# Kernel tuning notes

Measured on AMD Instinct MI355X. Metric: run time of the kernel, lower is better.

Reference implementation:

```python
import jax, jax.numpy as jnp
import numpy as np

B, T, C = 1, 2048, 1024
HS = 64
H = C // HS
EPS_GN = 0.00064


def _fwd(x, v_first, x_prev, init_state, x_r, x_w, x_k, x_v, x_a, x_g,
         w0, w1, w2, a0, a1, a2, v0, v1, v2, g1, g2,
         k_k, k_a, r_k, Wr, Wk, Wv, Wo, ln_w, ln_b, cu_seqlens):
    # token shift: previous token, sequence starts replaced by cached state x_prev
    xx = jnp.concatenate([jnp.zeros((1, 1, C), x.dtype), x[:, :-1, :]], axis=1)
    xx = xx.at[0, cu_seqlens[:-1], :].set(x_prev)
    xx = xx - x
    xr = x + xx * x_r
    xw = x + xx * x_w
    xk = x + xx * x_k
    xv = x + xx * x_v
    xa = x + xx * x_a
    xg = x + xx * x_g
    r = xr @ Wr.T
    # log-decay, strictly negative: w = -exp(-softplus(-z) - 0.5)
    w = -jnp.exp(-jax.nn.softplus(-(w0 + jnp.tanh(xw @ w1) @ w2)) - 0.5)
    k = xk @ Wk.T
    v = xv @ Wv.T
    # layer_id != 0: mix toward first-layer value
    v = v + (v_first - v) * jax.nn.sigmoid(v0 + (xv @ v1) @ v2)
    a = jax.nn.sigmoid(a0 + (xa @ a1) @ a2)
    g = jax.nn.sigmoid(xg @ g1) @ g2
    kk = (k * k_k).reshape(B, T, H, HS)
    kk = kk / jnp.maximum(jnp.linalg.norm(kk, axis=-1, keepdims=True), 1e-12)
    k = k * (1.0 + (a - 1.0) * k_a)
    r4 = r.reshape(B, T, H, HS)
    w4 = w.reshape(B, T, H, HS)
    k4 = k.reshape(B, T, H, HS)
    v4 = v.reshape(B, T, H, HS)
    a4 = a.reshape(B, T, H, HS)
    aa = -kk
    bb = kk * a4

    # RWKV-7 selective-decay linear RNN (chunk_rwkv7 semantics):
    #   S_t = S_{t-1} diag(exp(w_t)) + (S_{t-1} a_t) b_t^T + v_t k_t^T ; o_t = S_t r_t
    def step(S, ts):
        r_t, w_t, k_t, v_t, a_t, b_t = ts  # each [H,HS]
        sa = jnp.einsum('hvj,hj->hv', S, a_t)
        S = S * jnp.exp(w_t)[:, None, :] + sa[:, :, None] * b_t[:, None, :] \
            + v_t[:, :, None] * k_t[:, None, :]
        o = jnp.einsum('hvk,hk->hv', S, r_t)
        return S, o

    _, y = jax.lax.scan(step, init_state, (r4[0], w4[0], k4[0], v4[0], aa[0], bb[0]))
    # GroupNorm with num_groups=H over channels, eps=0.00064
    y = y.reshape(B * T, H, HS)
    mu = y.mean(-1, keepdims=True)
    var = ((y - mu) ** 2).mean(-1, keepdims=True)
    yn = (y - mu) / jnp.sqrt(var + EPS_GN)
    yn = yn * ln_w.reshape(H, HS) + ln_b.reshape(H, HS)
    xo = yn.reshape(B, T, C)
    # per-head bonus term
    xo = xo + ((r4 * k4 * r_k).sum(-1, keepdims=True) * v4).reshape(B, T, C)
    return (xo * g) @ Wo.T


def setup_inputs():
    keys = jax.random.split(jax.random.key(0), 32)
    it = iter(range(32))
    def nrm(shape, s=0.02):
        return jax.random.normal(keys[next(it)], shape, dtype=jnp.float32) * s
    inp = {}
    inp['x'] = jax.random.normal(keys[next(it)], (B, T, C), jnp.float32)
    inp['v_first'] = jax.random.normal(keys[next(it)], (B, T, C), jnp.float32)
    inp['x_prev'] = jax.random.normal(keys[next(it)], (1, C), jnp.float32)
    inp['init_state'] = jnp.zeros((H, HS, HS), jnp.float32)
    for nm in ['x_r', 'x_w', 'x_k', 'x_v', 'x_a', 'x_g', 'w0', 'a0', 'v0', 'k_k', 'k_a']:
        inp[nm] = nrm((C,))
    inp['w1'] = nrm((C, 64)); inp['w2'] = nrm((64, C))
    inp['a1'] = nrm((C, 64)); inp['a2'] = nrm((64, C))
    inp['v1'] = nrm((C, 32)); inp['v2'] = nrm((32, C))
    inp['g1'] = nrm((C, 128)); inp['g2'] = nrm((128, C))
    inp['r_k'] = nrm((H, HS))
    inp['Wr'] = nrm((C, C)); inp['Wk'] = nrm((C, C))
    inp['Wv'] = nrm((C, C)); inp['Wo'] = nrm((C, C))
    inp['ln_w'] = jnp.ones((C,), jnp.float32)
    inp['ln_b'] = jnp.zeros((C,), jnp.float32)
    inp['cu_seqlens'] = jnp.array([0, T], dtype=jnp.int32)
    return inp


def reference(x, v_first, x_prev, init_state, x_r, x_w, x_k, x_v, x_a, x_g,
              w0, w1, w2, a0, a1, a2, v0, v1, v2, g1, g2,
              k_k, k_a, r_k, Wr, Wk, Wv, Wo, ln_w, ln_b, cu_seqlens):
    return _fwd(x, v_first, x_prev, init_state, x_r, x_w, x_k, x_v, x_a, x_g,
                w0, w1, w2, a0, a1, a2, v0, v1, v2, g1, g2,
                k_k, k_a, r_k, Wr, Wk, Wv, Wo, ln_w, ln_b, cu_seqlens)
```

## Files before the change

kernel.cpp:

```cpp
#include <hip/hip_runtime.h>

#define T_LEN 2048
#define C_DIM 1024
#define PAIR_F 768
#define NCH 32
#define CPAIR 32

#define AS1 __attribute__((address_space(1)))
#define AS3 __attribute__((address_space(3)))

typedef __attribute__((ext_vector_type(8))) short bf8_t;
typedef __attribute__((ext_vector_type(4))) float f4_t;
typedef __attribute__((ext_vector_type(2))) float f2_t;

static __device__ __forceinline__ float sigf(float x) {
    return 1.f / (1.f + __expf(-x));
}
static __device__ __forceinline__ unsigned short f2bf(float f) {
    unsigned u = __float_as_uint(f);
    u += 0x7fff + ((u >> 16) & 1);
    return (unsigned short)(u >> 16);
}

static __device__ __forceinline__ float red16(float x) {
    int xi;
    xi = __builtin_amdgcn_mov_dpp(__float_as_int(x), 0x128, 0xf, 0xf, true);
    x += __int_as_float(xi);
    xi = __builtin_amdgcn_mov_dpp(__float_as_int(x), 0x124, 0xf, 0xf, true);
    x += __int_as_float(xi);
    xi = __builtin_amdgcn_mov_dpp(__float_as_int(x), 0x122, 0xf, 0xf, true);
    x += __int_as_float(xi);
    xi = __builtin_amdgcn_mov_dpp(__float_as_int(x), 0x121, 0xf, 0xf, true);
    x += __int_as_float(xi);
    return x;
}
static __device__ __forceinline__ float red64(float x) {
    x = red16(x);
    x += __shfl_xor(x, 16);
    x += __shfl_xor(x, 32);
    return x;
}

static __device__ __forceinline__ f2_t f2bc(float s) { return (f2_t){s, s}; }
static __device__ __forceinline__ f2_t fma2(f2_t a, f2_t b, f2_t c) {
    return __builtin_elementwise_fma(a, b, c);
}
static __device__ __forceinline__ f2_t lo2(const float4& v) { return (f2_t){v.x, v.y}; }
static __device__ __forceinline__ f2_t hi2(const float4& v) { return (f2_t){v.z, v.w}; }

static __device__ __forceinline__ float dot4pk(f2_t Sl, f2_t Sh, const float4& A) {
    f2_t m = Sl * lo2(A);
    m = fma2(Sh, hi2(A), m);
    return m.x + m.y;
}

__global__ __launch_bounds__(256) void wcvtall(
    const float* __restrict__ Wr, const float* __restrict__ Wk,
    const float* __restrict__ Wv, const float* __restrict__ Wo,
    const float* __restrict__ w1, const float* __restrict__ a1,
    const float* __restrict__ v1, const float* __restrict__ g1,
    unsigned short* __restrict__ dst, unsigned short* __restrict__ lw16)
{
    const int b = blockIdx.x;
    if (b < 4096) {
        const size_t idx = ((size_t)b * 256 + threadIdx.x) * 4;
        const int sel = (int)(idx >> 20);
        const float* src = sel == 0 ? Wr : sel == 1 ? Wk : sel == 2 ? Wv : Wo;
        float4 v = *(const float4*)(src + (idx & 0xFFFFF));
        ushort4 o = {f2bf(v.x), f2bf(v.y), f2bf(v.z), f2bf(v.w)};
        *(ushort4*)(dst + idx) = o;
        return;
    }
    const int row = b - 4096;
    const float* src; int Kh, i; unsigned short* dl;
    if (row < 64)       { src = w1; Kh = 64;  i = row;       dl = lw16 + (size_t)row * 1024; }
    else if (row < 128) { src = a1; Kh = 64;  i = row - 64;  dl = lw16 + (size_t)row * 1024; }
    else if (row < 160) { src = v1; Kh = 32;  i = row - 128; dl = lw16 + (size_t)(row - 128 + 128) * 1024; }
    else                { src = g1; Kh = 128; i = row - 160; dl = lw16 + (size_t)(row - 160 + 192) * 1024; }
    const int c0 = threadIdx.x * 4;
#pragma unroll
    for (int u = 0; u < 4; ++u)
        dl[c0 + u] = f2bf(src[(size_t)(c0 + u) * Kh + i]);
}

__global__ __launch_bounds__(256) void xcvt(
    const float* __restrict__ x, const float* __restrict__ xprev,
    const float* __restrict__ x_r, const float* __restrict__ x_k,
    const float* __restrict__ x_v, const float* __restrict__ x_w,
    const float* __restrict__ x_a, const float* __restrict__ x_g,
    unsigned short* __restrict__ xr16, unsigned short* __restrict__ xk16,
    unsigned short* __restrict__ xv16, unsigned short* __restrict__ xw16,
    unsigned short* __restrict__ xa16, unsigned short* __restrict__ xg16)
{
    const int t = blockIdx.x;
    const int c0 = threadIdx.x * 4;
    const size_t base = (size_t)t * C_DIM + c0;
    float4 xv = *(const float4*)(x + base);
    float4 pv = (t == 0) ? *(const float4*)(xprev + c0)
                         : *(const float4*)(x + base - C_DIM);
    float4 dx = {pv.x - xv.x, pv.y - xv.y, pv.z - xv.z, pv.w - xv.w};
#define MIXOUT(mixp, dstp)                                                    \
    {                                                                          \
        float4 mv = *(const float4*)(mixp + c0);                               \
        ushort4 o = {f2bf(xv.x + dx.x * mv.x), f2bf(xv.y + dx.y * mv.y),       \
                     f2bf(xv.z + dx.z * mv.z), f2bf(xv.w + dx.w * mv.w)};      \
        *(ushort4*)(dstp + base) = o;                                          \
    }
    MIXOUT(x_r, xr16) MIXOUT(x_k, xk16) MIXOUT(x_v, xv16)
    MIXOUT(x_w, xw16) MIXOUT(x_a, xa16) MIXOUT(x_g, xg16)
#undef MIXOUT
}

static __device__ __forceinline__ void gemm_core(
    const unsigned short* __restrict__ A, const unsigned short* __restrict__ W,
    float* __restrict__ out)
{
    __shared__ unsigned short Ab[2][128 * 32];
    __shared__ unsigned short Bb[2][64 * 32];
    const int tid = threadIdx.x;
    const int lane = tid & 63;
    const int w = tid >> 6;
    const int n0 = blockIdx.x * 64;
    const int t0 = blockIdx.y * 128;
    const int wm = (w & 1) * 64;
    const int wn = (w >> 1) * 32;
    const int srow = lane >> 2;
    const int scol = (lane & 3) * 8;

    f4_t acc[4][2];
#pragma unroll
    for (int i = 0; i < 4; ++i)
#pragma unroll
        for (int j = 0; j < 2; ++j)
            acc[i][j] = (f4_t){0.f, 0.f, 0.f, 0.f};

#pragma unroll
    for (int s = 0; s < 2; ++s) {
        const int i = 2 * w + s;
        __builtin_amdgcn_global_load_lds(
            (const AS1 unsigned int*)(A + (size_t)(t0 + i * 16 + srow) * 1024 + scol),
            (AS3 unsigned int*)(&Ab[0][i * 512 + lane * 8]), 16, 0, 0);
    }
    __builtin_amdgcn_global_load_lds(
        (const AS1 unsigned int*)(W + (size_t)(n0 + w * 16 + srow) * 1024 + scol),
        (AS3 unsigned int*)(&Bb[0][w * 512 + lane * 8]), 16, 0, 0);

    const int mrow = lane & 15;
    const int kq = (lane >> 4) * 8;
    for (int k0 = 0; k0 < 1024; k0 += 32) {
        const int cur = (k0 >> 5) & 1, nxt = cur ^ 1;
        __syncthreads();
        if (k0 + 32 < 1024) {
            const int k1 = k0 + 32;
#pragma unroll
            for (int s = 0; s < 2; ++s) {
                const int i = 2 * w + s;
                __builtin_amdgcn_global_load_lds(
                    (const AS1 unsigned int*)(A + (size_t)(t0 + i * 16 + srow) * 1024 + k1 + scol),
                    (AS3 unsigned int*)(&Ab[nxt][i * 512 + lane * 8]), 16, 0, 0);
            }
            __builtin_amdgcn_global_load_lds(
                (const AS1 unsigned int*)(W + (size_t)(n0 + w * 16 + srow) * 1024 + k1 + scol),
                (AS3 unsigned int*)(&Bb[nxt][w * 512 + lane * 8]), 16, 0, 0);
        }
        bf8_t af[4], bfr[2];
#pragma unroll
        for (int i = 0; i < 4; ++i)
            af[i] = *(const bf8_t*)(&Ab[cur][(wm + 16 * i + mrow) * 32 + kq]);
#pragma unroll
        for (int j = 0; j < 2; ++j)
            bfr[j] = *(const bf8_t*)(&Bb[cur][(wn + 16 * j + mrow) * 32 + kq]);
#pragma unroll
        for (int i = 0; i < 4; ++i)
#pragma unroll
            for (int j = 0; j < 2; ++j)
                acc[i][j] = __builtin_amdgcn_mfma_f32_16x16x32_bf16(
                    af[i], bfr[j], acc[i][j], 0, 0, 0);
    }
    const int crow = (lane >> 4) * 4;
    const int ccol = lane & 15;
#pragma unroll
    for (int i = 0; i < 4; ++i)
#pragma unroll
        for (int j = 0; j < 2; ++j)
#pragma unroll
            for (int u = 0; u < 4; ++u)
                out[(size_t)(t0 + wm + 16 * i + crow + u) * 1024
                    + n0 + wn + 16 * j + ccol] = acc[i][j][u];
}

__global__ __launch_bounds__(256) void gemm_bf16_3(
    const unsigned short* __restrict__ xr, const unsigned short* __restrict__ xk,
    const unsigned short* __restrict__ xv,
    const unsigned short* __restrict__ Wr, const unsigned short* __restrict__ Wk,
    const unsigned short* __restrict__ Wv,
    float* __restrict__ rB, float* __restrict__ kB, float* __restrict__ vB)
{
    const int z = blockIdx.z;
    const unsigned short* A = z == 0 ? xr : z == 1 ? xk : xv;
    const unsigned short* W = z == 0 ? Wr : z == 1 ? Wk : Wv;
    float* out = z == 0 ? rB : z == 1 ? kB : vB;
    gemm_core(A, W, out);
}

__global__ __launch_bounds__(256) void gemm_bf16(
    const unsigned short* __restrict__ A, const unsigned short* __restrict__ W,
    float* __restrict__ out)
{
    gemm_core(A, W, out);
}

__global__ __launch_bounds__(256) void lora1m(
    const unsigned short* __restrict__ xw, const unsigned short* __restrict__ xa,
    const unsigned short* __restrict__ xv, const unsigned short* __restrict__ xg,
    const unsigned short* __restrict__ lw16,
    float* __restrict__ hw, float* __restrict__ ha, float* __restrict__ hv,
    float* __restrict__ hg)
{
    const int z = blockIdx.z;
    const unsigned short* A = z == 0 ? xw : z == 1 ? xa : z == 2 ? xv : xg;
    const unsigned short* W = lw16 + (size_t)(z == 0 ? 0 : z == 1 ? 64 : z == 2 ? 128 : 192) * 1024;
    float* out = z == 0 ? hw : z == 1 ? ha : z == 2 ? hv : hg;
    const int N  = z == 3 ? 128 : z == 2 ? 32 : 64;
    const int Ns = z == 3 ? 128 : 64;
    const int n0 = blockIdx.x * 64;
    if (n0 >= Ns) return;

    __shared__ unsigned short Ab[2][128 * 32];
    __shared__ unsigned short Bb[2][64 * 32];
    const int tid = threadIdx.x;
    const int lane = tid & 63;
    const int w = tid >> 6;
    const int t0 = blockIdx.y * 128;
    const int wm = (w & 1) * 64;
    const int wn = (w >> 1) * 32;
    const int srow = lane >> 2;
    const int scol = (lane & 3) * 8;

    f4_t acc[4][2];
#pragma unroll
    for (int i = 0; i < 4; ++i)
#pragma unroll
        for (int j = 0; j < 2; ++j)
            acc[i][j] = (f4_t){0.f, 0.f, 0.f, 0.f};

#pragma unroll
    for (int s = 0; s < 2; ++s) {
        const int i = 2 * w + s;
        __builtin_amdgcn_global_load_lds(
            (const AS1 unsigned int*)(A + (size_t)(t0 + i * 16 + srow) * 1024 + scol),
            (AS3 unsigned int*)(&Ab[0][i * 512 + lane * 8]), 16, 0, 0);
    }
    __builtin_amdgcn_global_load_lds(
        (const AS1 unsigned int*)(W + (size_t)(n0 + w * 16 + srow) * 1024 + scol),
        (AS3 unsigned int*)(&Bb[0][w * 512 + lane * 8]), 16, 0, 0);

    const int mrow = lane & 15;
    const int kq = (lane >> 4) * 8;
    for (int k0 = 0; k0 < 1024; k0 += 32) {
        const int cur = (k0 >> 5) & 1, nxt = cur ^ 1;
        __syncthreads();
        if (k0 + 32 < 1024) {
            const int k1 = k0 + 32;
#pragma unroll
            for (int s = 0; s < 2; ++s) {
                const int i = 2 * w + s;
                __builtin_amdgcn_global_load_lds(
                    (const AS1 unsigned int*)(A + (size_t)(t0 + i * 16 + srow) * 1024 + k1 + scol),
                    (AS3 unsigned int*)(&Ab[nxt][i * 512 + lane * 8]), 16, 0, 0);
            }
            __builtin_amdgcn_global_load_lds(
                (const AS1 unsigned int*)(W + (size_t)(n0 + w * 16 + srow) * 1024 + k1 + scol),
                (AS3 unsigned int*)(&Bb[nxt][w * 512 + lane * 8]), 16, 0, 0);
        }
        bf8_t af[4], bfr[2];
#pragma unroll
        for (int i = 0; i < 4; ++i)
            af[i] = *(const bf8_t*)(&Ab[cur][(wm + 16 * i + mrow) * 32 + kq]);
#pragma unroll
        for (int j = 0; j < 2; ++j)
            bfr[j] = *(const bf8_t*)(&Bb[cur][(wn + 16 * j + mrow) * 32 + kq]);
#pragma unroll
        for (int i = 0; i < 4; ++i)
#pragma unroll
            for (int j = 0; j < 2; ++j)
                acc[i][j] = __builtin_amdgcn_mfma_f32_16x16x32_bf16(
                    af[i], bfr[j], acc[i][j], 0, 0, 0);
    }
    const int crow = (lane >> 4) * 4;
    const int ccol = lane & 15;
#pragma unroll
    for (int i = 0; i < 4; ++i)
#pragma unroll
        for (int j = 0; j < 2; ++j) {
            const int col = n0 + wn + 16 * j + ccol;
            if (col < N) {
#pragma unroll
                for (int u = 0; u < 4; ++u) {
                    float vv = acc[i][j][u];
                    if (z == 0) vv = tanhf(vv);
                    else if (z == 3) vv = sigf(vv);
                    out[(size_t)(t0 + wm + 16 * i + crow + u) * N + col] = vv;
                }
            }
        }
}

#define TOK 4
__global__ __launch_bounds__(256) void lora2f(
    const float* __restrict__ hwB, const float* __restrict__ haB,
    const float* __restrict__ hvB, const float* __restrict__ hgB,
    const float* __restrict__ w2, const float* __restrict__ a2,
    const float* __restrict__ v2, const float* __restrict__ g2,
    const float* __restrict__ w0, const float* __restrict__ a0,
    const float* __restrict__ v0,
    const float* __restrict__ k_k, const float* __restrict__ k_a,
    const float* __restrict__ v_first, const float* __restrict__ rB,
    float* __restrict__ kB, float* __restrict__ vB, float* __restrict__ gB,
    float* __restrict__ pk)
{
    const int tid = threadIdx.x;
    const int t0 = blockIdx.y * TOK;
    const int i  = blockIdx.x * 256 + tid;
    const int h  = i >> 6;
    const int j  = i & 63;

    float av[TOK], ew[TOK], vf[TOK];
    {
        float acc[TOK];
        const float b0 = a0[i];
#pragma unroll
        for (int tt = 0; tt < TOK; ++tt) acc[tt] = b0;
        for (int jj = 0; jj < 64; jj += 4) {
            const float q0 = a2[(size_t)(jj + 0) * C_DIM + i];
            const float q1 = a2[(size_t)(jj + 1) * C_DIM + i];
            const float q2 = a2[(size_t)(jj + 2) * C_DIM + i];
            const float q3 = a2[(size_t)(jj + 3) * C_DIM + i];
#pragma unroll
            for (int tt = 0; tt < TOK; ++tt) {
                float4 h4 = *(const float4*)(haB + (size_t)(t0 + tt) * 64 + jj);
                acc[tt] = fmaf(h4.x, q0, acc[tt]);
                acc[tt] = fmaf(h4.y, q1, acc[tt]);
                acc[tt] = fmaf(h4.z, q2, acc[tt]);
                acc[tt] = fmaf(h4.w, q3, acc[tt]);
            }
        }
#pragma unroll
        for (int tt = 0; tt < TOK; ++tt) av[tt] = sigf(acc[tt]);
    }
    {
        float acc[TOK];
        const float b0 = w0[i];
#pragma unroll
        for (int tt = 0; tt < TOK; ++tt) acc[tt] = b0;
        for (int jj = 0; jj < 64; jj += 4) {
            const float q0 = w2[(size_t)(jj + 0) * C_DIM + i];
            const float q1 = w2[(size_t)(jj + 1) * C_DIM + i];
            const float q2 = w2[(size_t)(jj + 2) * C_DIM + i];
            const float q3 = w2[(size_t)(jj + 3) * C_DIM + i];
#pragma unroll
            for (int tt = 0; tt < TOK; ++tt) {
                float4 h4 = *(const float4*)(hwB + (size_t)(t0 + tt) * 64 + jj);
                acc[tt] = fmaf(h4.x, q0, acc[tt]);
                acc[tt] = fmaf(h4.y, q1, acc[tt]);
                acc[tt] = fmaf(h4.z, q2, acc[tt]);
                acc[tt] = fmaf(h4.w, q3, acc[tt]);
            }
        }
#pragma unroll
        for (int tt = 0; tt < TOK; ++tt)
            ew[tt] = __expf(-0.6065306597126334f * sigf(acc[tt]));
    }
    {
        float acc[TOK];
        const float b0 = v0[i];
#pragma unroll
        for (int tt = 0; tt < TOK; ++tt) acc[tt] = b0;
        for (int jj = 0; jj < 32; jj += 4) {
            const float q0 = v2[(size_t)(jj + 0) * C_DIM + i];
            const float q1 = v2[(size_t)(jj + 1) * C_DIM + i];
            const float q2 = v2[(size_t)(jj + 2) * C_DIM + i];
            const float q3 = v2[(size_t)(jj + 3) * C_DIM + i];
#pragma unroll
            for (int tt = 0; tt < TOK; ++tt) {
                float4 h4 = *(const float4*)(hvB + (size_t)(t0 + tt) * 32 + jj);
                acc[tt] = fmaf(h4.x, q0, acc[tt]);
                acc[tt] = fmaf(h4.y, q1, acc[tt]);
                acc[tt] = fmaf(h4.z, q2, acc[tt]);
                acc[tt] = fmaf(h4.w, q3, acc[tt]);
            }
        }
#pragma unroll
        for (int tt = 0; tt < TOK; ++tt) {
            const size_t gi = (size_t)(t0 + tt) * C_DIM + i;
            const float s = sigf(acc[tt]);
            const float vr = vB[gi];
            vf[tt] = vr + (v_first[gi] - vr) * s;
            vB[gi] = vf[tt];
        }
    }
    {
        float acc[TOK];
#pragma unroll
        for (int tt = 0; tt < TOK; ++tt) acc[tt] = 0.f;
        for (int jj = 0; jj < 128; jj += 4) {
            const float q0 = g2[(size_t)(jj + 0) * C_DIM + i];
            const float q1 = g2[(size_t)(jj + 1) * C_DIM + i];
            const float q2 = g2[(size_t)(jj + 2) * C_DIM + i];
            const float q3 = g2[(size_t)(jj + 3) * C_DIM + i];
#pragma unroll
            for (int tt = 0; tt < TOK; ++tt) {
                float4 h4 = *(const float4*)(hgB + (size_t)(t0 + tt) * 128 + jj);
                acc[tt] = fmaf(h4.x, q0, acc[tt]);
                acc[tt] = fmaf(h4.y, q1, acc[tt]);
                acc[tt] = fmaf(h4.z, q2, acc[tt]);
                acc[tt] = fmaf(h4.w, q3, acc[tt]);
            }
        }
#pragma unroll
        for (int tt = 0; tt < TOK; ++tt)
            gB[(size_t)(t0 + tt) * C_DIM + i] = acc[tt];
    }
    const float kkw = k_k[i], kaw = k_a[i];
    const size_t pbase = (size_t)h * 1024 * PAIR_F;
    for (int pt = 0; pt < TOK / 2; ++pt) {
        float r_[2], e_[2], kf_[2], v_[2], aa_[2], bb_[2];
#pragma unroll
        for (int u = 0; u < 2; ++u) {
            const int tt = 2 * pt + u;
            const size_t gi = (size_t)(t0 + tt) * C_DIM + i;
            const float kraw = kB[gi];
            const float kn = kraw * kkw;
            const float ss = red64(kn * kn);
            const float sc = 1.f / fmaxf(sqrtf(ss), 1e-12f);
            const float kk = kn * sc;
            const float a_ = av[tt];
            const float kf = kraw * (1.f + (a_ - 1.f) * kaw);
            kB[gi] = kf;
            r_[u] = rB[gi];
            e_[u] = ew[tt];
            kf_[u] = kf;
            v_[u] = vf[tt];
            aa_[u] = -kk;
            bb_[u] = kk * a_;
        }
        const float E   = e_[0] * e_[1];
        const float A2e = e_[0] * aa_[1];
        const float B1e = bb_[0] * e_[1];
        const float K1e = kf_[0] * e_[1];
        const float R1e = e_[0] * r_[0];
        const float cba = red64(bb_[0] * aa_[1]);
        const float cka = red64(kf_[0] * aa_[1]);
        const float cbr = red64(bb_[0] * r_[0]);
        const float ckr = red64(kf_[0] * r_[0]);
        const float cbr2  = red64(B1e * r_[1]);
        const float ckr2  = red64(K1e * r_[1]);
        const float cb2r2 = red64(bb_[1] * r_[1]);
        const float ck2r2 = red64(kf_[1] * r_[1]);
        float* p = pk + pbase + (size_t)(blockIdx.y * (TOK / 2) + pt) * PAIR_F;
        p[j]        = E;
        p[64 + j]   = aa_[0];
        p[128 + j]  = A2e;
        p[192 + j]  = B1e;
        p[256 + j]  = K1e;
        p[320 + j]  = bb_[1];
        p[384 + j]  = kf_[1];
        p[448 + j]  = R1e;
        p[512 + j]  = E * r_[1];
        p[576 + 2 * j]     = v_[0];
        p[576 + 2 * j + 1] = v_[1];
        if (j == 0) {
            p[704] = cba;  p[705] = cka;  p[706] = cbr;  p[707] = ckr;
            p[708] = cbr2; p[709] = ckr2; p[710] = cb2r2; p[711] = ck2r2;
        }
    }
}

struct SlotPC {
    float4 E, A1, A2e, B1e, K1e, B2, K2;
    float4 vva, vvb;
    float4 sc;
};

static __device__ __forceinline__ void slot_load_pc(
    SlotPC& K, const float* __restrict__ p, int j0, int rb2)
{
    K.E   = *(const float4*)(p + j0);
    K.A1  = *(const float4*)(p + 64 + j0);
    K.A2e = *(const float4*)(p + 128 + j0);
    K.B1e = *(const float4*)(p + 192 + j0);
    K.K1e = *(const float4*)(p + 256 + j0);
    K.B2  = *(const float4*)(p + 320 + j0);
    K.K2  = *(const float4*)(p + 384 + j0);
    K.vva = *(const float4*)(p + 576 + rb2);
    K.vvb = *(const float4*)(p + 576 + rb2 + 4);
    K.sc  = *(const float4*)(p + 704);
}

static __device__ __forceinline__ void pair_pc(
    f2_t* PSl, f2_t* PSh, f2_t* CSl, f2_t* CSh, const SlotPC& K)
{
    float pu1[4], pu2[4], cu1[4], cu2[4];
#pragma unroll
    for (int r = 0; r < 4; ++r) {
        pu1[r] = red16(dot4pk(PSl[r], PSh[r], K.A1));
        pu2[r] = red16(dot4pk(PSl[r], PSh[r], K.A2e));
        cu1[r] = red16(dot4pk(CSl[r], CSh[r], K.A1));
        cu2[r] = red16(dot4pk(CSl[r], CSh[r], K.A2e));
    }
#pragma unroll
    for (int r = 0; r < 4; ++r) {
        {
            const float sa1 = pu1[r];
            const float sa2 = fmaf(sa1, K.sc.x, pu2[r]);
            const f2_t sa1v = f2bc(sa1), sa2v = f2bc(sa2);
            f2_t nl = PSl[r] * lo2(K.E), nh = PSh[r] * hi2(K.E);
            nl = fma2(sa1v, lo2(K.B1e), nl); nh = fma2(sa1v, hi2(K.B1e), nh);
            nl = fma2(sa2v, lo2(K.B2), nl);  nh = fma2(sa2v, hi2(K.B2), nh);
            PSl[r] = nl; PSh[r] = nh;
        }
        {
            const float v1 = r == 0 ? K.vva.x : r == 1 ? K.vva.z
                           : r == 2 ? K.vvb.x : K.vvb.z;
            const float v2 = r == 0 ? K.vva.y : r == 1 ? K.vva.w
                           : r == 2 ? K.vvb.y : K.vvb.w;
            const float sa1 = cu1[r];
            const float sa2 = fmaf(v1, K.sc.y, fmaf(sa1, K.sc.x, cu2[r]));
            const f2_t sa1v = f2bc(sa1), sa2v = f2bc(sa2);
            const f2_t v1v = f2bc(v1), v2v = f2bc(v2);
            f2_t nl = CSl[r] * lo2(K.E), nh = CSh[r] * hi2(K.E);
            nl = fma2(sa1v, lo2(K.B1e), nl); nh = fma2(sa1v, hi2(K.B1e), nh);
            nl = fma2(v1v, lo2(K.K1e), nl);  nh = fma2(v1v, hi2(K.K1e), nh);
            nl = fma2(sa2v, lo2(K.B2), nl);  nh = fma2(sa2v, hi2(K.B2), nh);
            nl = fma2(v2v, lo2(K.K2), nl);   nh = fma2(v2v, hi2(K.K2), nh);
            CSl[r] = nl; CSh[r] = nh;
        }
    }
}

__global__ __launch_bounds__(64, 1) void pc_fused(
    const float* __restrict__ pk, float* __restrict__ Pbuf,
    float* __restrict__ Cbuf)
{
    const int b = blockIdx.x;
    const int h = b & 15;
    const int w = (b >> 4) & 3;
    const int c = b >> 6;
    const int l = threadIdx.x;
    const int q = l >> 4;
    const int j0 = (l & 15) * 4;
    const int rbase = w * 16 + q * 4;
    const int rb2 = 2 * rbase;
    const float* hbase = pk + ((size_t)h * 1024 + (size_t)c * CPAIR) * PAIR_F;

    f2_t PSl[4], PSh[4], CSl[4], CSh[4];
#pragma unroll
    for (int r = 0; r < 4; ++r) {
        const int row = rbase + r;
        PSl[r] = (f2_t){j0 == row ? 1.f : 0.f, j0 + 1 == row ? 1.f : 0.f};
        PSh[r] = (f2_t){j0 + 2 == row ? 1.f : 0.f, j0 + 3 == row ? 1.f : 0.f};
        CSl[r] = (f2_t){0.f, 0.f};
        CSh[r] = (f2_t){0.f, 0.f};
    }

    SlotPC s0, s1, s2, s3;
    slot_load_pc(s0, hbase + 0 * PAIR_F, j0, rb2);
    slot_load_pc(s1, hbase + 1 * PAIR_F, j0, rb2);
    slot_load_pc(s2, hbase + 2 * PAIR_F, j0, rb2);
    slot_load_pc(s3, hbase + 3 * PAIR_F, j0, rb2);
    __builtin_amdgcn_sched_barrier(0);

    for (int i = 0; i < CPAIR - 4; i += 4) {
        const float* pl = hbase + (size_t)(i + 4) * PAIR_F;
        pair_pc(PSl, PSh, CSl, CSh, s0); slot_load_pc(s0, pl + 0 * PAIR_F, j0, rb2);
        __builtin_amdgcn_sched_barrier(0);
        pair_pc(PSl, PSh, CSl, CSh, s1); slot_load_pc(s1, pl + 1 * PAIR_F, j0, rb2);
        __builtin_amdgcn_sched_barrier(0);
        pair_pc(PSl, PSh, CSl, CSh, s2); slot_load_pc(s2, pl + 2 * PAIR_F, j0, rb2);
        __builtin_amdgcn_sched_barrier(0);
        pair_pc(PSl, PSh, CSl, CSh, s3); slot_load_pc(s3, pl + 3 * PAIR_F, j0, rb2);
        __builtin_amdgcn_sched_barrier(0);
    }
    pair_pc(PSl, PSh, CSl, CSh, s0);
    pair_pc(PSl, PSh, CSl, CSh, s1);
    pair_pc(PSl, PSh, CSl, CSh, s2);
    pair_pc(PSl, PSh, CSl, CSh, s3);

    const size_t cb64 = ((size_t)h * NCH + c) * 4096;
#pragma unroll
    for (int r = 0; r < 4; ++r) {
        *(float4*)(Pbuf + cb64 + (size_t)(rbase + r) * 64 + j0) =
            (float4){PSl[r].x, PSl[r].y, PSh[r].x, PSh[r].y};
        *(float4*)(Cbuf + cb64 + (size_t)(rbase + r) * 64 + j0) =
            (float4){CSl[r].x, CSl[r].y, CSh[r].x, CSh[r].y};
    }
}

__global__ __launch_bounds__(64) void combine(
    const float* __restrict__ Pbuf, float* __restrict__ CSbuf,
    const float* __restrict__ init_state)
{
    const int b = blockIdx.x;
    const int h = b & 15;
    const int g = b >> 4;
    const int l = threadIdx.x;
    const int vl = l >> 4;
    const int vidx = g * 4 + vl;
    const int j0 = (l & 15) * 4;
    __shared__ __align__(16) float Pl[64 * 64];
    __shared__ __align__(16) float sl[4 * 64];

    float4 s = *(const float4*)(init_state + h * 4096 + vidx * 64 + j0);
    for (int c = 0; c < NCH; ++c) {
        const size_t cbase = ((size_t)h * NCH + c) * 4096;
        float* cp = CSbuf + cbase + (size_t)vidx * 64 + j0;
        float4 Cv = *(const float4*)cp;
        *(float4*)cp = s;
        const float* Psrc = Pbuf + cbase;
#pragma unroll
        for (int t = 0; t < 16; ++t)
            *(float4*)(&Pl[t * 256 + l * 4]) = *(const float4*)(Psrc + t * 256 + l * 4);
        *(float4*)(&sl[vl * 64 + j0]) = s;
        __syncthreads();
        f2_t al = {Cv.x, Cv.y}, ah = {Cv.z, Cv.w};
        for (int k = 0; k < 64; ++k) {
            const float sk = sl[vl * 64 + k];
            float4 Pr = *(const float4*)(&Pl[k * 64 + j0]);
            al = fma2(f2bc(sk), lo2(Pr), al);
            ah = fma2(f2bc(sk), hi2(Pr), ah);
        }
        s = (float4){al.x, al.y, ah.x, ah.y};
        __syncthreads();
    }
}

struct SlotO {
    float4 E, A1, A2e, B1e, K1e, B2, K2, R1e, R2e;
    float4 vva, vvb;
    float4 sc, sc2;
};

static __device__ __forceinline__ void slot_load_o(
    SlotO& K, const float* __restrict__ p, int j0, int rb2)
{
    K.E   = *(const float4*)(p + j0);
    K.A1  = *(const float4*)(p + 64 + j0);
    K.A2e = *(const float4*)(p + 128 + j0);
    K.B1e = *(const float4*)(p + 192 + j0);
    K.K1e = *(const float4*)(p + 256 + j0);
    K.B2  = *(const float4*)(p + 320 + j0);
    K.K2  = *(const float4*)(p + 384 + j0);
    K.R1e = *(const float4*)(p + 448 + j0);
    K.R2e = *(const float4*)(p + 512 + j0);
    K.vva = *(const float4*)(p + 576 + rb2);
    K.vvb = *(const float4*)(p + 576 + rb2 + 4);
    K.sc  = *(const float4*)(p + 704);
    K.sc2 = *(const float4*)(p + 708);
}

static __device__ __forceinline__ void pair_out(
    f2_t* Sl, f2_t* Sh, const SlotO& K, float4& o1v, float4& o2v)
{
    float u1[4], u2[4], op[4], oz[4];
#pragma unroll
    for (int r = 0; r < 4; ++r) {
        u1[r] = red16(dot4pk(Sl[r], Sh[r], K.A1));
        u2[r] = red16(dot4pk(Sl[r], Sh[r], K.A2e));
        op[r] = red16(dot4pk(Sl[r], Sh[r], K.R1e));
        oz[r] = red16(dot4pk(Sl[r], Sh[r], K.R2e));
    }
    float o1a[4], o2a[4];
#pragma unroll
    for (int r = 0; r < 4; ++r) {
        const float v1 = r == 0 ? K.vva.x : r == 1 ? K.vva.z
                       : r == 2 ? K.vvb.x : K.vvb.z;
        const float v2 = r == 0 ? K.vva.y : r == 1 ? K.vva.w
                       : r == 2 ? K.vvb.y : K.vvb.w;
        const float sa1 = u1[r];
        const float sa2 = fmaf(v1, K.sc.y, fmaf(sa1, K.sc.x, u2[r]));
        o1a[r] = fmaf(v1, K.sc.w, fmaf(sa1, K.sc.z, op[r]));
        o2a[r] = fmaf(v2, K.sc2.w, fmaf(sa2, K.sc2.z,
                 fmaf(v1, K.sc2.y, fmaf(sa1, K.sc2.x, oz[r]))));
        const f2_t sa1v = f2bc(sa1), sa2v = f2bc(sa2);
        const f2_t v1v = f2bc(v1), v2v = f2bc(v2);
        f2_t nl = Sl[r] * lo2(K.E), nh = Sh[r] * hi2(K.E);
        nl = fma2(sa1v, lo2(K.B1e), nl); nh = fma2(sa1v, hi2(K.B1e), nh);
        nl = fma2(v1v, lo2(K.K1e), nl);  nh = fma2(v1v, hi2(K.K1e), nh);
        nl = fma2(sa2v, lo2(K.B2), nl);  nh = fma2(sa2v, hi2(K.B2), nh);
        nl = fma2(v2v, lo2(K.K2), nl);   nh = fma2(v2v, hi2(K.K2), nh);
        Sl[r] = nl; Sh[r] = nh;
    }
    o1v = (float4){o1a[0], o1a[1], o1a[2], o1a[3]};
    o2v = (float4){o2a[0], o2a[1], o2a[2], o2a[3]};
}

__global__ __launch_bounds__(64, 1) void out_scan(
    const float* __restrict__ pk, const float* __restrict__ Scbuf,
    float* __restrict__ y)
{
    const int b = blockIdx.x;
    const int h = b & 15;
    const int w = (b >> 4) & 3;
    const int c = b >> 6;
    const int l = threadIdx.x;
    const int q = l >> 4;
    const int j0 = (l & 15) * 4;
    const int rbase = w * 16 + q * 4;
    const int rb2 = 2 * rbase;
    const int cb = h * 64;
    const float* hbase = pk + ((size_t)h * 1024 + (size_t)c * CPAIR) * PAIR_F;
    const size_t cb64 = ((size_t)h * NCH + c) * 4096;

    f2_t Sl[4], Sh[4];
#pragma unroll
    for (int r = 0; r < 4; ++r) {
        float4 S4 = *(const float4*)(Scbuf + cb64 + (size_t)(rbase + r) * 64 + j0);
        Sl[r] = (f2_t){S4.x, S4.y};
        Sh[r] = (f2_t){S4.z, S4.w};
    }

    SlotO s0, s1;
    slot_load_o(s0, hbase + 0 * PAIR_F, j0, rb2);
    slot_load_o(s1, hbase + 1 * PAIR_F, j0, rb2);
    __builtin_amdgcn_sched_barrier(0);

    const bool wr = (l & 15) == 0;
    const int pi0 = c * CPAIR;
    float4 o1v, o2v;
#define OUT_STORE(pidx)                                                       \
    if (wr) {                                                                 \
        float* yp = y + (size_t)(2 * (pidx)) * C_DIM + cb + rbase;            \
        *(float4*)yp = o1v;                                                   \
        *(float4*)(yp + C_DIM) = o2v;                                         \
    }
    for (int i = 0; i < CPAIR - 2; i += 2) {
        pair_out(Sl, Sh, s0, o1v, o2v);
        slot_load_o(s0, hbase + (size_t)(i + 2) * PAIR_F, j0, rb2);
        __builtin_amdgcn_sched_barrier(0);
        OUT_STORE(pi0 + i)
        pair_out(Sl, Sh, s1, o1v, o2v);
        if (i + 3 < CPAIR)
            slot_load_o(s1, hbase + (size_t)(i + 3) * PAIR_F, j0, rb2);
        __builtin_amdgcn_sched_barrier(0);
        OUT_STORE(pi0 + i + 1)
    }
    pair_out(Sl, Sh, s0, o1v, o2v);
    OUT_STORE(pi0 + CPAIR - 2)
    pair_out(Sl, Sh, s1, o1v, o2v);
    OUT_STORE(pi0 + CPAIR - 1)
#undef OUT_STORE
}

__global__ __launch_bounds__(256) void gn_bonus(
    const float* __restrict__ y, const float* __restrict__ rb,
    const float* __restrict__ kb, const float* __restrict__ vb,
    const float* __restrict__ gb, const float* __restrict__ r_k,
    const float* __restrict__ lnw, const float* __restrict__ lnb,
    unsigned short* __restrict__ yg)
{
    const int t = blockIdx.x, tid = threadIdx.x;
    const int c0 = tid << 2;
    const size_t base = (size_t)t * C_DIM + c0;
    float4 yv = *(const float4*)(y + base);
    float sum = yv.x + yv.y + yv.z + yv.w;
    float ss  = yv.x * yv.x + yv.y * yv.y + yv.z * yv.z + yv.w * yv.w;
    float4 rv = *(const float4*)(rb + base);
    float4 kv = *(const float4*)(kb + base);
    float4 rkv = *(const float4*)(r_k + c0);
    float dot = rv.x * kv.x * rkv.x + rv.y * kv.y * rkv.y +
                rv.z * kv.z * rkv.z + rv.w * kv.w * rkv.w;
#pragma unroll
    for (int m = 1; m <= 8; m <<= 1) {
        sum += __shfl_xor(sum, m);
        ss  += __shfl_xor(ss, m);
        dot += __shfl_xor(dot, m);
    }
    const float mu = sum * 0.015625f;
    const float var = ss * 0.015625f - mu * mu;
    const float rstd = rsqrtf(var + 0.00064f);
    float4 wv = *(const float4*)(lnw + c0);
    float4 bv = *(const float4*)(lnb + c0);
    float4 vv = *(const float4*)(vb + base);
    float4 gv = *(const float4*)(gb + base);
    ushort4 o;
    o.x = f2bf(((yv.x - mu) * rstd * wv.x + bv.x + dot * vv.x) * gv.x);
    o.y = f2bf(((yv.y - mu) * rstd * wv.y + bv.y + dot * vv.y) * gv.y);
    o.z = f2bf(((yv.z - mu) * rstd * wv.z + bv.z + dot * vv.z) * gv.z);
    o.w = f2bf(((yv.w - mu) * rstd * wv.w + bv.w + dot * vv.w) * gv.w);
    *(ushort4*)(yg + base) = o;
}

extern "C" void kernel_launch(void* const* d_in, const int* in_sizes, int n_in,
                              void* d_out, int out_size, void* d_ws, size_t ws_size,
                              hipStream_t stream)
{
    (void)in_sizes; (void)n_in; (void)out_size; (void)ws_size;
    const float* x       = (const float*)d_in[0];
    const float* v_first = (const float*)d_in[1];
    const float* x_prev  = (const float*)d_in[2];
    const float* init_st = (const float*)d_in[3];
    const float* x_r = (const float*)d_in[4];
    const float* x_w = (const float*)d_in[5];
    const float* x_k = (const float*)d_in[6];
    const float* x_v = (const float*)d_in[7];
    const float* x_a = (const float*)d_in[8];
    const float* x_g = (const float*)d_in[9];
    const float* w0  = (const float*)d_in[10];
    const float* a0  = (const float*)d_in[11];
    const float* v0  = (const float*)d_in[12];
    const float* k_k = (const float*)d_in[13];
    const float* k_a = (const float*)d_in[14];
    const float* w1  = (const float*)d_in[15];
    const float* w2  = (const float*)d_in[16];
    const float* a1  = (const float*)d_in[17];
    const float* a2  = (const float*)d_in[18];
    const float* v1  = (const float*)d_in[19];
    const float* v2  = (const float*)d_in[20];
    const float* g1  = (const float*)d_in[21];
    const float* g2  = (const float*)d_in[22];
    const float* r_k = (const float*)d_in[23];
    const float* Wr  = (const float*)d_in[24];
    const float* Wk  = (const float*)d_in[25];
    const float* Wv  = (const float*)d_in[26];
    const float* Wo  = (const float*)d_in[27];
    const float* ln_w = (const float*)d_in[28];
    const float* ln_b = (const float*)d_in[29];

    float* out = (float*)d_out;
    float* ws  = (float*)d_ws;
    const size_t NE = (size_t)T_LEN * C_DIM;
    const size_t WE = (size_t)C_DIM * C_DIM;
    float* rB  = ws;
    float* kB  = ws + NE;
    float* vB  = ws + 2 * NE;
    float* gB  = ws + 3 * NE;
    float* hwB = ws + 4 * NE;
    float* haB = hwB + (size_t)T_LEN * 64;
    float* hvB = haB + (size_t)T_LEN * 64;
    float* hgB = hvB + (size_t)T_LEN * 32;
    float* pk  = ws + 4 * NE + NE / 2;
    unsigned short* b16 = (unsigned short*)(ws + 10 * NE + NE / 2);
    unsigned short* xr16 = b16;
    unsigned short* xk16 = b16 + NE;
    unsigned short* xv16 = b16 + 2 * NE;
    unsigned short* Wr16 = b16 + 3 * NE;
    unsigned short* Wk16 = Wr16 + WE;
    unsigned short* Wv16 = Wr16 + 2 * WE;
    unsigned short* Wo16 = Wr16 + 3 * WE;
    unsigned short* yg16 = b16 + 3 * NE + 4 * WE;
    unsigned short* lw16 = yg16 + NE;
    unsigned short* xw16 = (unsigned short*)pk;
    unsigned short* xa16 = xw16 + NE;
    unsigned short* xg16 = xw16 + 2 * NE;
    float* yB = (float*)xr16;
    float* Pbuf  = (float*)xr16;
    float* CSbuf = (float*)xv16;

    wcvtall<<<4384, 256, 0, stream>>>(Wr, Wk, Wv, Wo, w1, a1, v1, g1,
                                      Wr16, lw16);
    xcvt<<<T_LEN, 256, 0, stream>>>(x, x_prev, x_r, x_k, x_v, x_w, x_a, x_g,
                                    xr16, xk16, xv16, xw16, xa16, xg16);

    gemm_bf16_3<<<dim3(16, 16, 3), 256, 0, stream>>>(
        xr16, xk16, xv16, Wr16, Wk16, Wv16, rB, kB, vB);

    lora1m<<<dim3(2, 16, 4), 256, 0, stream>>>(
        xw16, xa16, xv16, xg16, lw16, hwB, haB, hvB, hgB);

    lora2f<<<dim3(4, T_LEN / TOK), 256, 0, stream>>>(
        hwB, haB, hvB, hgB, w2, a2, v2, g2, w0, a0, v0,
        k_k, k_a, v_first, rB, kB, vB, gB, pk);

    pc_fused<<<16 * 4 * NCH, 64, 0, stream>>>(pk, Pbuf, CSbuf);
    combine<<<256, 64, 0, stream>>>(Pbuf, CSbuf, init_st);
    out_scan<<<16 * 4 * NCH, 64, 0, stream>>>(pk, CSbuf, yB);

    gn_bonus<<<T_LEN, 256, 0, stream>>>(yB, rB, kB, vB, gB, r_k, ln_w, ln_b, yg16);
    gemm_bf16<<<dim3(16, 16), 256, 0, stream>>>(yg16, Wo16, out);
}
```

Measured before the change: 378.2 us.

## Move g-LoRA second projection from scalar FMA loop to bf16 MFMA GEMM

The sigmoid(xg@g1)@g2 projection is taken out of the fp32 scalar loop in lora2f and computed by a new bf16 MFMA GEMM kernel (K=128). lora1m now writes the hidden activation in bf16, and wcvtall gains extra blocks that transpose g2 and convert it to bf16. This cuts scalar FMA work and g2 reloads in lora2f, at the cost of one more kernel launch and bf16 rounding of the gate path.

```diff
diff --git a/kernel.cpp b/kernel.cpp
--- a/kernel.cpp
+++ b/kernel.cpp
@@ -59,7 +59,9 @@
     const float* __restrict__ Wv, const float* __restrict__ Wo,
     const float* __restrict__ w1, const float* __restrict__ a1,
     const float* __restrict__ v1, const float* __restrict__ g1,
-    unsigned short* __restrict__ dst, unsigned short* __restrict__ lw16)
+    const float* __restrict__ g2,
+    unsigned short* __restrict__ dst, unsigned short* __restrict__ lw16,
+    unsigned short* __restrict__ g2t16)
 {
     const int b = blockIdx.x;
     if (b < 4096) {
@@ -69,6 +71,13 @@
         float4 v = *(const float4*)(src + (idx & 0xFFFFF));
         ushort4 o = {f2bf(v.x), f2bf(v.y), f2bf(v.z), f2bf(v.w)};
         *(ushort4*)(dst + idx) = o;
+        return;
+    }
+    if (b >= 4384) {
+        const int rr = b - 4384;
+        const int i  = rr * 2 + (threadIdx.x >> 7);
+        const int c  = threadIdx.x & 127;
+        g2t16[(size_t)i * 128 + c] = f2bf(g2[(size_t)c * C_DIM + i]);
         return;
     }
     const int row = b - 4096;
@@ -210,17 +219,95 @@
     gemm_core(A, W, out);
 }
 
+__global__ __launch_bounds__(256) void gemm_g(
+    const unsigned short* __restrict__ A, const unsigned short* __restrict__ W,
+    float* __restrict__ out)
+{
+    __shared__ unsigned short Ab[2][128 * 32];
+    __shared__ unsigned short Bb[2][64 * 32];
+    const int tid = threadIdx.x;
+    const int lane = tid & 63;
+    const int w = tid >> 6;
+    const int n0 = blockIdx.x * 64;
+    const int t0 = blockIdx.y * 128;
+    const int wm = (w & 1) * 64;
+    const int wn = (w >> 1) * 32;
+    const int srow = lane >> 2;
+    const int scol = (lane & 3) * 8;
+
+    f4_t acc[4][2];
+#pragma unroll
+    for (int i = 0; i < 4; ++i)
+#pragma unroll
+        for (int j = 0; j < 2; ++j)
+            acc[i][j] = (f4_t){0.f, 0.f, 0.f, 0.f};
+
+#pragma unroll
+    for (int s = 0; s < 2; ++s) {
+        const int i = 2 * w + s;
+        __builtin_amdgcn_global_load_lds(
+            (const AS1 unsigned int*)(A + (size_t)(t0 + i * 16 + srow) * 128 + scol),
+            (AS3 unsigned int*)(&Ab[0][i * 512 + lane * 8]), 16, 0, 0);
+    }
+    __builtin_amdgcn_global_load_lds(
+        (const AS1 unsigned int*)(W + (size_t)(n0 + w * 16 + srow) * 128 + scol),
+        (AS3 unsigned int*)(&Bb[0][w * 512 + lane * 8]), 16, 0, 0);
+
+    const int mrow = lane & 15;
+    const int kq = (lane >> 4) * 8;
+    for (int k0 = 0; k0 < 128; k0 += 32) {
+        const int cur = (k0 >> 5) & 1, nxt = cur ^ 1;
+        __syncthreads();
+        if (k0 + 32 < 128) {
+            const int k1 = k0 + 32;
+#pragma unroll
+            for (int s = 0; s < 2; ++s) {
+                const int i = 2 * w + s;
+                __builtin_amdgcn_global_load_lds(
+                    (const AS1 unsigned int*)(A + (size_t)(t0 + i * 16 + srow) * 128 + k1 + scol),
+                    (AS3 unsigned int*)(&Ab[nxt][i * 512 + lane * 8]), 16, 0, 0);
+            }
+            __builtin_amdgcn_global_load_lds(
+                (const AS1 unsigned int*)(W + (size_t)(n0 + w * 16 + srow) * 128 + k1 + scol),
+                (AS3 unsigned int*)(&Bb[nxt][w * 512 + lane * 8]), 16, 0, 0);
+        }
+        bf8_t af[4], bfr[2];
+#pragma unroll
+        for (int i = 0; i < 4; ++i)
+            af[i] = *(const bf8_t*)(&Ab[cur][(wm + 16 * i + mrow) * 32 + kq]);
+#pragma unroll
+        for (int j = 0; j < 2; ++j)
+            bfr[j] = *(const bf8_t*)(&Bb[cur][(wn + 16 * j + mrow) * 32 + kq]);
+#pragma unroll
+        for (int i = 0; i < 4; ++i)
+#pragma unroll
+            for (int j = 0; j < 2; ++j)
+                acc[i][j] = __builtin_amdgcn_mfma_f32_16x16x32_bf16(
+                    af[i], bfr[j], acc[i][j], 0, 0, 0);
+    }
+    const int crow = (lane >> 4) * 4;
+    const int ccol = lane & 15;
+#pragma unroll
+    for (int i = 0; i < 4; ++i)
+#pragma unroll
+        for (int j = 0; j < 2; ++j)
+#pragma unroll
+            for (int u = 0; u < 4; ++u)
+                out[(size_t)(t0 + wm + 16 * i + crow + u) * 1024
+                    + n0 + wn + 16 * j + ccol] = acc[i][j][u];
+}
+
 __global__ __launch_bounds__(256) void lora1m(
     const unsigned short* __restrict__ xw, const unsigned short* __restrict__ xa,
     const unsigned short* __restrict__ xv, const unsigned short* __restrict__ xg,
     const unsigned short* __restrict__ lw16,
     float* __restrict__ hw, float* __restrict__ ha, float* __restrict__ hv,
-    float* __restrict__ hg)
+    unsigned short* __restrict__ hg16)
 {
     const int z = blockIdx.z;
     const unsigned short* A = z == 0 ? xw : z == 1 ? xa : z == 2 ? xv : xg;
     const unsigned short* W = lw16 + (size_t)(z == 0 ? 0 : z == 1 ? 64 : z == 2 ? 128 : 192) * 1024;
-    float* out = z == 0 ? hw : z == 1 ? ha : z == 2 ? hv : hg;
+    float* out = z == 0 ? hw : z == 1 ? ha : hv;
     const int N  = z == 3 ? 128 : z == 2 ? 32 : 64;
     const int Ns = z == 3 ? 128 : 64;
     const int n0 = blockIdx.x * 64;
@@ -298,9 +385,15 @@
 #pragma unroll
                 for (int u = 0; u < 4; ++u) {
                     float vv = acc[i][j][u];
-                    if (z == 0) vv = tanhf(vv);
-                    else if (z == 3) vv = sigf(vv);
-                    out[(size_t)(t0 + wm + 16 * i + crow + u) * N + col] = vv;
+                    if (z == 0) {
+                        vv = tanhf(vv);
+                        out[(size_t)(t0 + wm + 16 * i + crow + u) * N + col] = vv;
+                    } else if (z == 3) {
+                        vv = sigf(vv);
+                        hg16[(size_t)(t0 + wm + 16 * i + crow + u) * 128 + col] = f2bf(vv);
+                    } else {
+                        out[(size_t)(t0 + wm + 16 * i + crow + u) * N + col] = vv;
+                    }
                 }
             }
         }
@@ -309,14 +402,14 @@
 #define TOK 4
 __global__ __launch_bounds__(256) void lora2f(
     const float* __restrict__ hwB, const float* __restrict__ haB,
-    const float* __restrict__ hvB, const float* __restrict__ hgB,
+    const float* __restrict__ hvB,
     const float* __restrict__ w2, const float* __restrict__ a2,
-    const float* __restrict__ v2, const float* __restrict__ g2,
+    const float* __restrict__ v2,
     const float* __restrict__ w0, const float* __restrict__ a0,
     const float* __restrict__ v0,
     const float* __restrict__ k_k, const float* __restrict__ k_a,
     const float* __restrict__ v_first, const float* __restrict__ rB,
-    float* __restrict__ kB, float* __restrict__ vB, float* __restrict__ gB,
+    float* __restrict__ kB, float* __restrict__ vB,
     float* __restrict__ pk)
 {
     const int tid = threadIdx.x;
@@ -398,28 +491,6 @@
             vf[tt] = vr + (v_first[gi] - vr) * s;
             vB[gi] = vf[tt];
         }
-    }
-    {
-        float acc[TOK];
-#pragma unroll
-        for (int tt = 0; tt < TOK; ++tt) acc[tt] = 0.f;
-        for (int jj = 0; jj < 128; jj += 4) {
-            const float q0 = g2[(size_t)(jj + 0) * C_DIM + i];
-            const float q1 = g2[(size_t)(jj + 1) * C_DIM + i];
-            const float q2 = g2[(size_t)(jj + 2) * C_DIM + i];
-            const float q3 = g2[(size_t)(jj + 3) * C_DIM + i];
-#pragma unroll
-            for (int tt = 0; tt < TOK; ++tt) {
-                float4 h4 = *(const float4*)(hgB + (size_t)(t0 + tt) * 128 + jj);
-                acc[tt] = fmaf(h4.x, q0, acc[tt]);
-                acc[tt] = fmaf(h4.y, q1, acc[tt]);
-                acc[tt] = fmaf(h4.z, q2, acc[tt]);
-                acc[tt] = fmaf(h4.w, q3, acc[tt]);
-            }
-        }
-#pragma unroll
-        for (int tt = 0; tt < TOK; ++tt)
-            gB[(size_t)(t0 + tt) * C_DIM + i] = acc[tt];
     }
     const float kkw = k_k[i], kaw = k_a[i];
     const size_t pbase = (size_t)h * 1024 * PAIR_F;
@@ -837,7 +908,6 @@
     float* hwB = ws + 4 * NE;
     float* haB = hwB + (size_t)T_LEN * 64;
     float* hvB = haB + (size_t)T_LEN * 64;
-    float* hgB = hvB + (size_t)T_LEN * 32;
     float* pk  = ws + 4 * NE + NE / 2;
     unsigned short* b16 = (unsigned short*)(ws + 10 * NE + NE / 2);
     unsigned short* xr16 = b16;
@@ -849,6 +919,8 @@
     unsigned short* Wo16 = Wr16 + 3 * WE;
     unsigned short* yg16 = b16 + 3 * NE + 4 * WE;
     unsigned short* lw16 = yg16 + NE;
+    unsigned short* hg16 = lw16 + (size_t)320 * 1024;
+    unsigned short* g2t16 = hg16 + (size_t)T_LEN * 128;
     unsigned short* xw16 = (unsigned short*)pk;
     unsigned short* xa16 = xw16 + NE;
     unsigned short* xg16 = xw16 + 2 * NE;
@@ -856,8 +928,8 @@
     float* Pbuf  = (float*)xr16;
     float* CSbuf = (float*)xv16;
 
-    wcvtall<<<4384, 256, 0, stream>>>(Wr, Wk, Wv, Wo, w1, a1, v1, g1,
-                                      Wr16, lw16);
+    wcvtall<<<4896, 256, 0, stream>>>(Wr, Wk, Wv, Wo, w1, a1, v1, g1, g2,
+                                      Wr16, lw16, g2t16);
     xcvt<<<T_LEN, 256, 0, stream>>>(x, x_prev, x_r, x_k, x_v, x_w, x_a, x_g,
                                     xr16, xk16, xv16, xw16, xa16, xg16);
 
@@ -865,11 +937,13 @@
         xr16, xk16, xv16, Wr16, Wk16, Wv16, rB, kB, vB);
 
     lora1m<<<dim3(2, 16, 4), 256, 0, stream>>>(
-        xw16, xa16, xv16, xg16, lw16, hwB, haB, hvB, hgB);
+        xw16, xa16, xv16, xg16, lw16, hwB, haB, hvB, hg16);
+
+    gemm_g<<<dim3(16, 16), 256, 0, stream>>>(hg16, g2t16, gB);
 
     lora2f<<<dim3(4, T_LEN / TOK), 256, 0, stream>>>(
-        hwB, haB, hvB, hgB, w2, a2, v2, g2, w0, a0, v0,
-        k_k, k_a, v_first, rB, kB, vB, gB, pk);
+        hwB, haB, hvB, w2, a2, v2, w0, a0, v0,
+        k_k, k_a, v_first, rB, kB, vB, pk);
 
     pc_fused<<<16 * 4 * NCH, 64, 0, stream>>>(pk, Pbuf, CSbuf);
     combine<<<256, 64, 0, stream>>>(Pbuf, CSbuf, init_st);
```

After: 369.4 us. 1.02x faster.
